# Kernel tuning notes

Measured on AMD Instinct MI355X. Metric: run time of the kernel, lower is better.

The kernel has to match this reference:

```python
import math
import jax, jax.numpy as jnp
import numpy as np
from jax import lax

B, T, D_HEAD, M_FEAT = 8, 8192, 64, 256
EPS = 1e-6


def _draw_omega(key, d, m):
    # Orthogonal random features: QR blocks of size d x d, rows rescaled by
    # the Frobenius row-norms of the original Gaussian blocks (chi scaling).
    n_blocks = math.ceil(m / d)
    blocks = []
    for i in range(n_blocks):
        g = jax.random.normal(jax.random.fold_in(key, i), (d, d), dtype=jnp.float32)
        qb, _ = jnp.linalg.qr(g)
        norms = jnp.linalg.norm(g, axis=1)
        blocks.append(qb * norms[:, None])
    return jnp.concatenate(blocks, axis=0)[:m]


def setup_inputs() -> dict:
    key = jax.random.key(0)
    kq, kk, kv, ko = jax.random.split(key, 4)
    q = jax.random.normal(kq, (B, T, D_HEAD), dtype=jnp.float32)
    k = jax.random.normal(kk, (B, T, D_HEAD), dtype=jnp.float32)
    v = jax.random.normal(kv, (B, T, D_HEAD), dtype=jnp.float32)
    omega = _draw_omega(ko, D_HEAD, M_FEAT)
    return {"q": q, "k": k, "v": v, "omega": omega}


def _positive_map(x, omega):
    # phi(x) = exp(x @ omega^T - ||x||^2/2 - rowmax) / sqrt(m)
    log_phi = x @ omega.T - 0.5 * jnp.sum(x * x, axis=-1, keepdims=True)
    log_phi = log_phi - jnp.max(log_phi, axis=-1, keepdims=True)
    m = omega.shape[0]
    return jnp.exp(log_phi) / jnp.sqrt(jnp.asarray(m, dtype=x.dtype))


def reference(q, k, v, omega):
    scale = 1.0 / math.sqrt(q.shape[-1])
    phi_q = _positive_map(q * scale, omega)  # (B, T, m)
    phi_k = _positive_map(k * scale, omega)  # (B, T, m)

    def step(carry, xs):
        S, z = carry                     # S: (B, m, d), z: (B, m)
        pq, pk, vt = xs                  # each (B, m) / (B, m) / (B, d)
        S = S + pk[:, :, None] * vt[:, None, :]
        z = z + pk
        out = jnp.einsum('bm,bmd->bd', pq, S)
        denom = jnp.sum(pq * z, axis=-1, keepdims=True) + EPS
        return (S, z), out / denom

    S0 = jnp.zeros((q.shape[0], omega.shape[0], v.shape[-1]), dtype=q.dtype)
    z0 = jnp.zeros((q.shape[0], omega.shape[0]), dtype=q.dtype)
    xs = (jnp.swapaxes(phi_q, 0, 1), jnp.swapaxes(phi_k, 0, 1), jnp.swapaxes(v, 0, 1))
    _, outs = lax.scan(step, (S0, z0), xs)   # outs: (T, B, d)
    return jnp.swapaxes(outs, 0, 1)          # (B, T, d)
```

## Files before the change

### kernel.cpp

```cpp
#include <hip/hip_runtime.h>
#include <hip/hip_bf16.h>

typedef __hip_bfloat16 bf16;
typedef __attribute__((ext_vector_type(8))) short short8;
typedef __attribute__((ext_vector_type(4))) short shortx4;
typedef __attribute__((ext_vector_type(4))) float floatx4;

#define NEED_WS_BYTES 110625024ULL

__device__ __forceinline__ float b2f(bf16 x) { return __bfloat162float(x); }
__device__ __forceinline__ bf16  f2b(float x) { return __float2bfloat16(x); }
__device__ __forceinline__ float bflo(unsigned u) { return __uint_as_float(u << 16); }
__device__ __forceinline__ float bfhi(unsigned u) { return __uint_as_float(u & 0xffff0000u); }

__device__ __forceinline__ float ldin(const void* p, size_t i, int isf32) {
  return isf32 ? ((const float*)p)[i] : b2f(((const bf16*)p)[i]);
}

__device__ __forceinline__ short sb(float f) {
  bf16 h = f2b(f * 0.125f);
  return *reinterpret_cast<short*>(&h);
}
__device__ __forceinline__ short scale_b(short u) {
  float f = __uint_as_float(((unsigned)(unsigned short)u) << 16) * 0.125f;
  bf16 h = f2b(f);
  return *reinterpret_cast<short*>(&h);
}

__device__ __forceinline__ int detect_f32(const void* q, int tid, int* cntp) {
  if (tid == 0) *cntp = 0;
  __syncthreads();
  const unsigned short* u = (const unsigned short*)q;
  int c = 0;
  for (int e = tid; e < 2048; e += 256) {
    unsigned short w = u[2 * e];
    int ex = (w >> 7) & 0xFF;
    if ((w & 0x7FFF) != 0 && (ex < 110 || ex > 140)) c++;
  }
  atomicAdd(cntp, c);
  __syncthreads();
  return (*cntp > 512) ? 1 : 0;
}

__global__ __launch_bounds__(256) void k_omega(const void* __restrict__ q,
                                               const void* __restrict__ omega,
                                               bf16* __restrict__ omb,
                                               int* __restrict__ flag) {
  __shared__ int cnt;
  int tid = threadIdx.x;
  int isf32 = detect_f32(q, tid, &cnt);
  if (blockIdx.x == 0 && tid == 0) *flag = isf32;
  int e = blockIdx.x * 256 + tid;
  omb[e] = f2b(ldin(omega, e, isf32));
}

__device__ __forceinline__ void phi_load_a(const void* src, size_t row, int quad,
                                           int isf32, short8& a0, short8& a1) {
  if (isf32) {
    const float* xr = (const float*)src + row * 64;
    float4 f0 = *reinterpret_cast<const float4*>(xr + quad * 8);
    float4 f1 = *reinterpret_cast<const float4*>(xr + quad * 8 + 4);
    float4 f2 = *reinterpret_cast<const float4*>(xr + 32 + quad * 8);
    float4 f3 = *reinterpret_cast<const float4*>(xr + 32 + quad * 8 + 4);
    a0[0] = sb(f0.x); a0[1] = sb(f0.y); a0[2] = sb(f0.z); a0[3] = sb(f0.w);
    a0[4] = sb(f1.x); a0[5] = sb(f1.y); a0[6] = sb(f1.z); a0[7] = sb(f1.w);
    a1[0] = sb(f2.x); a1[1] = sb(f2.y); a1[2] = sb(f2.z); a1[3] = sb(f2.w);
    a1[4] = sb(f3.x); a1[5] = sb(f3.y); a1[6] = sb(f3.z); a1[7] = sb(f3.w);
  } else {
    const short* xr = (const short*)src + row * 64;
    short8 r0 = *reinterpret_cast<const short8*>(xr + quad * 8);
    short8 r1 = *reinterpret_cast<const short8*>(xr + 32 + quad * 8);
    #pragma unroll
    for (int j = 0; j < 8; ++j) { a0[j] = scale_b(r0[j]); a1[j] = scale_b(r1[j]); }
  }
}

__device__ __forceinline__ void stage_omb_lds(const bf16* __restrict__ omb,
                                              short* __restrict__ lds, int tid) {
  const short* src = (const short*)omb;
  #pragma unroll
  for (int it = 0; it < 8; ++it) {
    int seg = it * 256 + tid;
    int row = seg >> 3, s = seg & 7;
    *reinterpret_cast<short8*>(&lds[row * 64 + (s ^ (row & 7)) * 8]) =
        *reinterpret_cast<const short8*>(src + row * 64 + s * 8);
  }
}

__device__ __forceinline__ void phi_mfma_lds(const short* __restrict__ oml,
                                             int li, int quad,
                                             const short8& a0, const short8& a1,
                                             floatx4* c, float* mx) {
  int x = li & 7;
  #pragma unroll
  for (int n0 = 0; n0 < 16; ++n0) {
    const short* rp = oml + (n0 * 16 + li) * 64;
    short8 b0 = *reinterpret_cast<const short8*>(rp + (quad ^ x) * 8);
    short8 b1 = *reinterpret_cast<const short8*>(rp + ((quad + 4) ^ x) * 8);
    floatx4 acc = {0.f, 0.f, 0.f, 0.f};
    acc = __builtin_amdgcn_mfma_f32_16x16x32_bf16(a0, b0, acc, 0, 0, 0);
    acc = __builtin_amdgcn_mfma_f32_16x16x32_bf16(a1, b1, acc, 0, 0, 0);
    c[n0] = acc;
  }
  #pragma unroll
  for (int r = 0; r < 4; ++r) {
    float m = c[0][r];
    #pragma unroll
    for (int n0 = 1; n0 < 16; ++n0) m = fmaxf(m, c[n0][r]);
    mx[r] = m;
  }
  #pragma unroll
  for (int mask = 1; mask < 16; mask <<= 1) {
    #pragma unroll
    for (int r = 0; r < 4; ++r) mx[r] = fmaxf(mx[r], __shfl_xor(mx[r], mask, 64));
  }
}

__global__ __launch_bounds__(256)
__attribute__((amdgpu_waves_per_eu(1, 3))) void k_phik(
    const void* __restrict__ k, const void* __restrict__ v,
    const bf16* __restrict__ omb, bf16* __restrict__ phiK,
    bf16* __restrict__ SlocT, float* __restrict__ zloc,
    const int* __restrict__ flag) {
  __shared__ short pkT[256 * 64];
  __shared__ short vTh[64 * 72];
  __shared__ short vTl[64 * 72];

  int isf32 = *flag;
  int tid = threadIdx.x;
  size_t tok0 = (size_t)blockIdx.x * 64;
  int li = tid & 15;
  int quad = (tid >> 4) & 3;
  int w = tid >> 6;
  int m0 = w * 16;
  size_t row = tok0 + m0 + li;

  stage_omb_lds(omb, pkT, tid);
  #pragma unroll
  for (int it = 0; it < 16; ++it) {
    int e = it * 256 + tid;
    int tau = e >> 6, d = e & 63;
    float vv = ldin(v, tok0 * 64 + e, isf32);
    bf16 h = f2b(vv);
    bf16 l = f2b(vv - b2f(h));
    vTh[d * 72 + tau] = *reinterpret_cast<short*>(&h);
    vTl[d * 72 + tau] = *reinterpret_cast<short*>(&l);
  }
  short8 a0, a1;
  phi_load_a(k, row, quad, isf32, a0, a1);

  __syncthreads();

  floatx4 c[16];
  float mx[4];
  phi_mfma_lds(pkT, li, quad, a0, a1, c, mx);

  __syncthreads();

  #pragma unroll
  for (int n0 = 0; n0 < 16; ++n0) {
    #pragma unroll
    for (int r = 0; r < 4; ++r) {
      bf16 hv = f2b(__expf(c[n0][r] - mx[r]) * 0.0625f);
      short hb = *reinterpret_cast<short*>(&hv);
      int i = n0 * 16 + li;
      int t = m0 + quad * 4 + r;
      ((short*)phiK)[(tok0 + t) * 256 + i] = hb;
      int cch = (t >> 3) ^ (i & 7);
      pkT[i * 64 + cch * 8 + (t & 7)] = hb;
    }
  }

  __syncthreads();

  {
    int i2 = tid;
    float zz = 0.f;
    #pragma unroll
    for (int c8 = 0; c8 < 8; ++c8) {
      short8 vv8 = *reinterpret_cast<const short8*>(
          &pkT[i2 * 64 + (c8 ^ (i2 & 7)) * 8]);
      #pragma unroll
      for (int j = 0; j < 8; ++j) zz += bflo((unsigned)(unsigned short)vv8[j]);
    }
    zloc[(size_t)blockIdx.x * 256 + i2] = zz;
  }

  int wbase = w * 64;
  floatx4 sa[4][4];
  #pragma unroll
  for (int mt = 0; mt < 4; ++mt)
    #pragma unroll
    for (int n0 = 0; n0 < 4; ++n0) sa[mt][n0] = (floatx4){0.f, 0.f, 0.f, 0.f};

  #pragma unroll
  for (int h = 0; h < 2; ++h) {
    short8 Ah[4], Al[4];
    #pragma unroll
    for (int mt = 0; mt < 4; ++mt) {
      Ah[mt] = *reinterpret_cast<const short8*>(
          &vTh[(mt * 16 + li) * 72 + h * 32 + quad * 8]);
      Al[mt] = *reinterpret_cast<const short8*>(
          &vTl[(mt * 16 + li) * 72 + h * 32 + quad * 8]);
    }
    #pragma unroll
    for (int n0 = 0; n0 < 4; ++n0) {
      int crow = wbase + n0 * 16 + li;
      int cc = (h * 4 + quad) ^ (li & 7);
      short8 Bq = *reinterpret_cast<const short8*>(&pkT[crow * 64 + cc * 8]);
      #pragma unroll
      for (int mt = 0; mt < 4; ++mt) {
        sa[mt][n0] =
            __builtin_amdgcn_mfma_f32_16x16x32_bf16(Ah[mt], Bq, sa[mt][n0], 0, 0, 0);
        sa[mt][n0] =
            __builtin_amdgcn_mfma_f32_16x16x32_bf16(Al[mt], Bq, sa[mt][n0], 0, 0, 0);
      }
    }
  }

  bf16* Sb = SlocT + (size_t)blockIdx.x * 16384;
  #pragma unroll
  for (int mt = 0; mt < 4; ++mt)
    #pragma unroll
    for (int n0 = 0; n0 < 4; ++n0)
      #pragma unroll
      for (int r = 0; r < 4; ++r)
        Sb[(mt * 16 + quad * 4 + r) * 256 + wbase + n0 * 16 + li] =
            f2b(sa[mt][n0][r]);
}

__global__ __launch_bounds__(256) void k_prefix(bf16* __restrict__ SlocT,
                                                float* __restrict__ zloc) {
  __shared__ float tot[4][64][2];
  int tid = threadIdx.x;
  int lane = tid & 63;
  int w = tid >> 6;
  if (blockIdx.x < 1024) {
    int b = blockIdx.x >> 7, g = blockIdx.x & 127;
    int p = g * 64 + lane;
    unsigned* base = (unsigned*)(SlocT + (size_t)b * 2097152) + p;
    unsigned vb[32];
    #pragma unroll
    for (int j = 0; j < 32; ++j) vb[j] = base[(size_t)(w * 32 + j) * 8192];
    float t0 = 0.f, t1 = 0.f;
    #pragma unroll
    for (int j = 0; j < 32; ++j) { t0 += bflo(vb[j]); t1 += bfhi(vb[j]); }
    tot[w][lane][0] = t0; tot[w][lane][1] = t1;
    __syncthreads();
    float r0 = 0.f, r1 = 0.f;
    for (int w2 = 0; w2 < w; ++w2) {
      r0 += tot[w2][lane][0]; r1 += tot[w2][lane][1];
    }
    #pragma unroll
    for (int j = 0; j < 32; ++j) {
      unsigned u = vb[j];
      bf16 h0 = f2b(r0), h1 = f2b(r1);
      unsigned pw = ((unsigned)*(unsigned short*)&h0) |
                    (((unsigned)*(unsigned short*)&h1) << 16);
      base[(size_t)(w * 32 + j) * 8192] = pw;
      r0 += bflo(u); r1 += bfhi(u);
    }
  } else {
    int idx = blockIdx.x - 1024;
    int b = idx >> 2, ig = idx & 3;
    int i = ig * 64 + lane;
    float* base = zloc + (size_t)b * 32768 + i;
    float vb[32];
    #pragma unroll
    for (int j = 0; j < 32; ++j) vb[j] = base[(size_t)(w * 32 + j) * 256];
    float t = 0.f;
    #pragma unroll
    for (int j = 0; j < 32; ++j) t += vb[j];
    tot[w][lane][0] = t;
    __syncthreads();
    float r = 0.f;
    for (int w2 = 0; w2 < w; ++w2) r += tot[w2][lane][0];
    #pragma unroll
    for (int j = 0; j < 32; ++j) {
      float tt = vb[j];
      base[(size_t)(w * 32 + j) * 256] = r;
      r += tt;
    }
  }
}

__global__ __launch_bounds__(256)
__attribute__((amdgpu_waves_per_eu(1, 3))) void k_out(
    const void* __restrict__ q, const bf16* __restrict__ omb,
    const bf16* __restrict__ phiK, const void* __restrict__ v,
    const bf16* __restrict__ SlocT, const float* __restrict__ zloc,
    void* __restrict__ outp, const int* __restrict__ flag) {
  __shared__ short spT[64 * 264];
  __shared__ short vTh[64 * 72];
  __shared__ short aT[64 * 72];

  int isf32 = *flag;
  int chunk = blockIdx.x;
  size_t tok0 = (size_t)chunk * 64;
  int tid = threadIdx.x;
  int lane = tid & 63;
  int li = lane & 15;
  int quad = lane >> 4;
  int w = __builtin_amdgcn_readfirstlane(tid >> 6);
  int m0 = w * 16;

  stage_omb_lds(omb, spT, tid);
  #pragma unroll
  for (int it = 0; it < 16; ++it) {
    int e = it * 256 + tid;
    int tau = e >> 6, d = e & 63;
    bf16 h = f2b(ldin(v, tok0 * 64 + e, isf32));
    vTh[d * 72 + tau] = *reinterpret_cast<short*>(&h);
  }
  {
    shortx4 z4 = {0, 0, 0, 0};
    int arow0 = m0 + li;
    for (int cc = (w + 1) * 16 + quad * 4; cc < 64; cc += 16)
      *reinterpret_cast<shortx4*>(&aT[arow0 * 72 + cc]) = z4;
  }
  short8 qa0, qa1;
  phi_load_a(q, tok0 + m0 + li, quad, isf32, qa0, qa1);

  __syncthreads();

  floatx4 c[16];
  float mx[4];
  phi_mfma_lds(spT, li, quad, qa0, qa1, c, mx);

  __syncthreads();

  float dpart[4] = {0.f, 0.f, 0.f, 0.f};
  {
    const float* zp = zloc + (size_t)chunk * 256;
    #pragma unroll
    for (int n0 = 0; n0 < 16; ++n0) {
      float zv = zp[n0 * 16 + li];
      #pragma unroll
      for (int r = 0; r < 4; ++r) {
        bf16 hv = f2b(__expf(c[n0][r] - mx[r]) * 0.0625f);
        short hb = *reinterpret_cast<short*>(&hv);
        spT[(m0 + quad * 4 + r) * 264 + n0 * 16 + li] = hb;
        dpart[r] += bflo((unsigned)(unsigned short)hb) * zv;
      }
    }
  }

  const short* pqf = &spT[(m0 + li) * 264 + quad * 8];
  short8 a1[8];
  #pragma unroll
  for (int kk = 0; kk < 8; ++kk)
    a1[kk] = *reinterpret_cast<const short8*>(pqf + kk * 32);

  __syncthreads();

  {
    const short* src = (const short*)phiK + tok0 * 256;
    #pragma unroll
    for (int it = 0; it < 8; ++it) {
      int e = it * 256 + tid;
      int tau = e >> 5, seg = e & 31;
      *reinterpret_cast<short8*>(&spT[tau * 264 + seg * 8]) =
          *reinterpret_cast<const short8*>(src + tau * 256 + seg * 8);
    }
  }

  __syncthreads();

  floatx4 c1[4];
  #pragma unroll
  for (int n0 = 0; n0 < 4; ++n0) c1[n0] = (floatx4){0.f, 0.f, 0.f, 0.f};
  #pragma unroll
  for (int n0 = 0; n0 < 4; ++n0) {
    if (n0 <= w) {
      const short* bp = &spT[(n0 * 16 + li) * 264 + quad * 8];
      floatx4 acc = c1[n0];
      #pragma unroll
      for (int kk = 0; kk < 8; ++kk) {
        short8 b = *reinterpret_cast<const short8*>(bp + kk * 32);
        acc = __builtin_amdgcn_mfma_f32_16x16x32_bf16(a1[kk], b, acc, 0, 0, 0);
      }
      c1[n0] = acc;
    }
  }

  #pragma unroll
  for (int n0 = 0; n0 < 4; ++n0) {
    if (n0 <= w) {
      int tau = n0 * 16 + li;
      #pragma unroll
      for (int r = 0; r < 4; ++r) {
        int t = m0 + quad * 4 + r;
        float val = (tau <= t) ? c1[n0][r] : 0.f;
        dpart[r] += val;
        bf16 hh = f2b(val);
        aT[t * 72 + tau] = *reinterpret_cast<short*>(&hh);
      }
    }
  }

  __syncthreads();

  {
    const short* src = (const short*)SlocT + (size_t)chunk * 16384;
    #pragma unroll
    for (int it = 0; it < 8; ++it) {
      int e = it * 256 + tid;
      int d = e >> 5, seg = e & 31;
      *reinterpret_cast<short8*>(&spT[d * 264 + seg * 8]) =
          *reinterpret_cast<const short8*>(src + d * 256 + seg * 8);
    }
  }

  __syncthreads();

  floatx4 o[4];
  #pragma unroll
  for (int n0 = 0; n0 < 4; ++n0) o[n0] = (floatx4){0.f, 0.f, 0.f, 0.f};

  const short* arow = &aT[(m0 + li) * 72 + quad * 8];
  short8 a3_0 = *reinterpret_cast<const short8*>(arow);
  short8 a3_1 = *reinterpret_cast<const short8*>(arow + 32);

  #pragma unroll
  for (int n0 = 0; n0 < 4; ++n0) {
    floatx4 acc = o[n0];
    const short* sp = &spT[(n0 * 16 + li) * 264 + quad * 8];
    #pragma unroll
    for (int kk = 0; kk < 8; ++kk) {
      short8 b = *reinterpret_cast<const short8*>(sp + kk * 32);
      acc = __builtin_amdgcn_mfma_f32_16x16x32_bf16(a1[kk], b, acc, 0, 0, 0);
    }
    const short* vph = &vTh[(n0 * 16 + li) * 72 + quad * 8];
    short8 bh0 = *reinterpret_cast<const short8*>(vph);
    short8 bh1 = *reinterpret_cast<const short8*>(vph + 32);
    acc = __builtin_amdgcn_mfma_f32_16x16x32_bf16(a3_0, bh0, acc, 0, 0, 0);
    acc = __builtin_amdgcn_mfma_f32_16x16x32_bf16(a3_1, bh1, acc, 0, 0, 0);
    o[n0] = acc;
  }

  #pragma unroll
  for (int mask = 1; mask < 16; mask <<= 1) {
    #pragma unroll
    for (int r = 0; r < 4; ++r) dpart[r] += __shfl_xor(dpart[r], mask, 64);
  }

  #pragma unroll
  for (int r = 0; r < 4; ++r) {
    float rd = 1.f / (dpart[r] + 1e-6f);
    size_t obb = (tok0 + m0 + quad * 4 + r) * 64 + li;
    if (isf32) {
      float* op = (float*)outp + obb;
      #pragma unroll
      for (int n0 = 0; n0 < 4; ++n0) op[n0 * 16] = o[n0][r] * rd;
    } else {
      bf16* op = (bf16*)outp + obb;
      #pragma unroll
      for (int n0 = 0; n0 < 4; ++n0) op[n0 * 16] = f2b(o[n0][r] * rd);
    }
  }
}

extern "C" void kernel_launch(void* const* d_in, const int* in_sizes, int n_in,
                              void* d_out, int out_size, void* d_ws, size_t ws_size,
                              hipStream_t stream) {
  (void)in_sizes; (void)n_in; (void)out_size;
  if (ws_size < NEED_WS_BYTES) return;

  const void* q = d_in[0];
  const void* k = d_in[1];
  const void* v = d_in[2];
  const void* omega = d_in[3];

  int*   flag = (int*)d_ws;
  float* wsf  = (float*)d_ws + 64;
  bf16*  omb  = (bf16*)wsf;
  float* zloc = wsf + 131072;
  bf16*  Sloc = (bf16*)(wsf + 393216);
  bf16*  phiK = (bf16*)(wsf + 17170432);

  k_omega<<<64, 256, 0, stream>>>(q, omega, omb, flag);
  k_phik<<<1024, 256, 0, stream>>>(k, v, omb, phiK, Sloc, zloc, flag);
  k_prefix<<<1056, 256, 0, stream>>>(Sloc, zloc);
  k_out<<<1024, 256, 0, stream>>>(q, omb, phiK, v, Sloc, zloc, d_out, flag);
}
```

Measured before the change: 160.0 us.

## Fuse omega conversion into phi kernels and drop split-bf16 V in chunk state

Removes the separate k_omega launch. Each block of k_phik and k_out now detects the input dtype itself and converts omega from the raw input straight into LDS. k_phik also drops the hi/lo bf16 split of V, halving the MFMAs and LDS traffic for the per-chunk state, and stores V in a swizzled LDS layout. Its waves-per-EU hint is raised. In exchange, every block repeats the dtype detection and omega conversion, and the local state sums lose precision without the low-order V term.

```diff
diff --git a/kernel.cpp b/kernel.cpp
--- a/kernel.cpp
+++ b/kernel.cpp
@@ -17,20 +17,20 @@
   return isf32 ? ((const float*)p)[i] : b2f(((const bf16*)p)[i]);
 }
 
-__device__ __forceinline__ short sb(float f) {
-  bf16 h = f2b(f * 0.125f);
-  return *reinterpret_cast<short*>(&h);
-}
-__device__ __forceinline__ short scale_b(short u) {
-  float f = __uint_as_float(((unsigned)(unsigned short)u) << 16) * 0.125f;
+__device__ __forceinline__ short tob(float f) {
   bf16 h = f2b(f);
   return *reinterpret_cast<short*>(&h);
 }
-
-__device__ __forceinline__ int detect_f32(const void* q, int tid, int* cntp) {
+__device__ __forceinline__ short sb(float f) { return tob(f * 0.125f); }
+__device__ __forceinline__ short scale_b(short u) {
+  return tob(__uint_as_float(((unsigned)(unsigned short)u) << 16) * 0.125f);
+}
+
+__device__ __forceinline__ int detect_f32_lds(const void* x, int tid,
+                                              int* cntp) {
   if (tid == 0) *cntp = 0;
   __syncthreads();
-  const unsigned short* u = (const unsigned short*)q;
+  const unsigned short* u = (const unsigned short*)x;
   int c = 0;
   for (int e = tid; e < 2048; e += 256) {
     unsigned short w = u[2 * e];
@@ -39,19 +39,38 @@
   }
   atomicAdd(cntp, c);
   __syncthreads();
-  return (*cntp > 512) ? 1 : 0;
-}
-
-__global__ __launch_bounds__(256) void k_omega(const void* __restrict__ q,
-                                               const void* __restrict__ omega,
-                                               bf16* __restrict__ omb,
-                                               int* __restrict__ flag) {
-  __shared__ int cnt;
-  int tid = threadIdx.x;
-  int isf32 = detect_f32(q, tid, &cnt);
-  if (blockIdx.x == 0 && tid == 0) *flag = isf32;
-  int e = blockIdx.x * 256 + tid;
-  omb[e] = f2b(ldin(omega, e, isf32));
+  int r = (*cntp > 512) ? 1 : 0;
+  __syncthreads();
+  return r;
+}
+
+__device__ __forceinline__ void stage_om_raw(const void* __restrict__ omega,
+                                             short* __restrict__ lds, int tid,
+                                             int isf32) {
+  if (isf32) {
+    const float* src = (const float*)omega;
+    #pragma unroll
+    for (int it = 0; it < 8; ++it) {
+      int seg = it * 256 + tid;
+      int row = seg >> 3, s = seg & 7;
+      const float* p = src + row * 64 + s * 8;
+      float4 f0 = *reinterpret_cast<const float4*>(p);
+      float4 f1 = *reinterpret_cast<const float4*>(p + 4);
+      short8 vv;
+      vv[0] = tob(f0.x); vv[1] = tob(f0.y); vv[2] = tob(f0.z); vv[3] = tob(f0.w);
+      vv[4] = tob(f1.x); vv[5] = tob(f1.y); vv[6] = tob(f1.z); vv[7] = tob(f1.w);
+      *reinterpret_cast<short8*>(&lds[row * 64 + (s ^ (row & 7)) * 8]) = vv;
+    }
+  } else {
+    const short* src = (const short*)omega;
+    #pragma unroll
+    for (int it = 0; it < 8; ++it) {
+      int seg = it * 256 + tid;
+      int row = seg >> 3, s = seg & 7;
+      *reinterpret_cast<short8*>(&lds[row * 64 + (s ^ (row & 7)) * 8]) =
+          *reinterpret_cast<const short8*>(src + row * 64 + s * 8);
+    }
+  }
 }
 
 __device__ __forceinline__ void phi_load_a(const void* src, size_t row, int quad,
@@ -75,18 +94,6 @@
   }
 }
 
-__device__ __forceinline__ void stage_omb_lds(const bf16* __restrict__ omb,
-                                              short* __restrict__ lds, int tid) {
-  const short* src = (const short*)omb;
-  #pragma unroll
-  for (int it = 0; it < 8; ++it) {
-    int seg = it * 256 + tid;
-    int row = seg >> 3, s = seg & 7;
-    *reinterpret_cast<short8*>(&lds[row * 64 + (s ^ (row & 7)) * 8]) =
-        *reinterpret_cast<const short8*>(src + row * 64 + s * 8);
-  }
-}
-
 __device__ __forceinline__ void phi_mfma_lds(const short* __restrict__ oml,
                                              int li, int quad,
                                              const short8& a0, const short8& a1,
@@ -117,16 +124,13 @@
 }
 
 __global__ __launch_bounds__(256)
-__attribute__((amdgpu_waves_per_eu(1, 3))) void k_phik(
+__attribute__((amdgpu_waves_per_eu(1, 4))) void k_phik(
     const void* __restrict__ k, const void* __restrict__ v,
-    const bf16* __restrict__ omb, bf16* __restrict__ phiK,
-    bf16* __restrict__ SlocT, float* __restrict__ zloc,
-    const int* __restrict__ flag) {
+    const void* __restrict__ omega, bf16* __restrict__ phiK,
+    bf16* __restrict__ SlocT, float* __restrict__ zloc) {
   __shared__ short pkT[256 * 64];
-  __shared__ short vTh[64 * 72];
-  __shared__ short vTl[64 * 72];
-
-  int isf32 = *flag;
+  __shared__ short vT[64 * 64];
+
   int tid = threadIdx.x;
   size_t tok0 = (size_t)blockIdx.x * 64;
   int li = tid & 15;
@@ -135,16 +139,15 @@
   int m0 = w * 16;
   size_t row = tok0 + m0 + li;
 
-  stage_omb_lds(omb, pkT, tid);
+  int isf32 = detect_f32_lds(k, tid, (int*)pkT);
+
+  stage_om_raw(omega, pkT, tid, isf32);
   #pragma unroll
   for (int it = 0; it < 16; ++it) {
     int e = it * 256 + tid;
     int tau = e >> 6, d = e & 63;
-    float vv = ldin(v, tok0 * 64 + e, isf32);
-    bf16 h = f2b(vv);
-    bf16 l = f2b(vv - b2f(h));
-    vTh[d * 72 + tau] = *reinterpret_cast<short*>(&h);
-    vTl[d * 72 + tau] = *reinterpret_cast<short*>(&l);
+    vT[d * 64 + (((tau >> 3) ^ (d & 7)) * 8) + (tau & 7)] =
+        tob(ldin(v, tok0 * 64 + e, isf32));
   }
   short8 a0, a1;
   phi_load_a(k, row, quad, isf32, a0, a1);
@@ -195,26 +198,20 @@
 
   #pragma unroll
   for (int h = 0; h < 2; ++h) {
-    short8 Ah[4], Al[4];
-    #pragma unroll
-    for (int mt = 0; mt < 4; ++mt) {
+    short8 Ah[4];
+    #pragma unroll
+    for (int mt = 0; mt < 4; ++mt)
       Ah[mt] = *reinterpret_cast<const short8*>(
-          &vTh[(mt * 16 + li) * 72 + h * 32 + quad * 8]);
-      Al[mt] = *reinterpret_cast<const short8*>(
-          &vTl[(mt * 16 + li) * 72 + h * 32 + quad * 8]);
-    }
+          &vT[(mt * 16 + li) * 64 + ((h * 4 + quad) ^ (li & 7)) * 8]);
     #pragma unroll
     for (int n0 = 0; n0 < 4; ++n0) {
       int crow = wbase + n0 * 16 + li;
       int cc = (h * 4 + quad) ^ (li & 7);
       short8 Bq = *reinterpret_cast<const short8*>(&pkT[crow * 64 + cc * 8]);
       #pragma unroll
-      for (int mt = 0; mt < 4; ++mt) {
+      for (int mt = 0; mt < 4; ++mt)
         sa[mt][n0] =
             __builtin_amdgcn_mfma_f32_16x16x32_bf16(Ah[mt], Bq, sa[mt][n0], 0, 0, 0);
-        sa[mt][n0] =
-            __builtin_amdgcn_mfma_f32_16x16x32_bf16(Al[mt], Bq, sa[mt][n0], 0, 0, 0);
-      }
     }
   }
 
@@ -286,15 +283,14 @@
 
 __global__ __launch_bounds__(256)
 __attribute__((amdgpu_waves_per_eu(1, 3))) void k_out(
-    const void* __restrict__ q, const bf16* __restrict__ omb,
+    const void* __restrict__ q, const void* __restrict__ omega,
     const bf16* __restrict__ phiK, const void* __restrict__ v,
     const bf16* __restrict__ SlocT, const float* __restrict__ zloc,
-    void* __restrict__ outp, const int* __restrict__ flag) {
+    void* __restrict__ outp) {
   __shared__ short spT[64 * 264];
   __shared__ short vTh[64 * 72];
   __shared__ short aT[64 * 72];
 
-  int isf32 = *flag;
   int chunk = blockIdx.x;
   size_t tok0 = (size_t)chunk * 64;
   int tid = threadIdx.x;
@@ -304,13 +300,14 @@
   int w = __builtin_amdgcn_readfirstlane(tid >> 6);
   int m0 = w * 16;
 
-  stage_omb_lds(omb, spT, tid);
+  int isf32 = detect_f32_lds(q, tid, (int*)spT);
+
+  stage_om_raw(omega, spT, tid, isf32);
   #pragma unroll
   for (int it = 0; it < 16; ++it) {
     int e = it * 256 + tid;
     int tau = e >> 6, d = e & 63;
-    bf16 h = f2b(ldin(v, tok0 * 64 + e, isf32));
-    vTh[d * 72 + tau] = *reinterpret_cast<short*>(&h);
+    vTh[d * 72 + tau] = tob(ldin(v, tok0 * 64 + e, isf32));
   }
   {
     shortx4 z4 = {0, 0, 0, 0};
@@ -471,15 +468,12 @@
   const void* v = d_in[2];
   const void* omega = d_in[3];
 
-  int*   flag = (int*)d_ws;
   float* wsf  = (float*)d_ws + 64;
-  bf16*  omb  = (bf16*)wsf;
   float* zloc = wsf + 131072;
   bf16*  Sloc = (bf16*)(wsf + 393216);
   bf16*  phiK = (bf16*)(wsf + 17170432);
 
-  k_omega<<<64, 256, 0, stream>>>(q, omega, omb, flag);
-  k_phik<<<1024, 256, 0, stream>>>(k, v, omb, phiK, Sloc, zloc, flag);
+  k_phik<<<1024, 256, 0, stream>>>(k, v, omega, phiK, Sloc, zloc);
   k_prefix<<<1056, 256, 0, stream>>>(Sloc, zloc);
-  k_out<<<1024, 256, 0, stream>>>(q, omb, phiK, v, Sloc, zloc, d_out, flag);
-}
+  k_out<<<1024, 256, 0, stream>>>(q, omega, phiK, v, Sloc, zloc, d_out);
+}
```

After: 168.3 us. 5.2% more time.
